# Optimization experiments

Hardware: AMD Instinct MI355X
Metric: run time of the kernel (lower is better)

Reference implementation:

```python
import jax, jax.numpy as jnp
import numpy as np

THETA = 10.0      # spike threshold
TAU_SR = 10.0     # synaptic (PSP) alpha-kernel time constant
TAU_REF = 1.0     # refractory alpha-kernel time constant
SCALE_REF = 2.0   # refractory scale (kernel = -scaleRef*theta*(t/tauRef)e^{1-t/tauRef})
TAU_RHO = 1.0     # surrogate-gradient width
SCALE_RHO = 1.0   # surrogate-gradient scale
TS = 1.0          # simulation step (ms)
E = 2.718281828459045

@jax.custom_vjp
def spike_surrogate(u):
    return (u >= THETA).astype(u.dtype)

def _spike_fwd(u):
    return (u >= THETA).astype(u.dtype), u

def _spike_bwd(u, g):
    # SLAYER surrogate spike-pdf gradient
    pdf = (SCALE_RHO / TAU_RHO) * jnp.exp(-jnp.abs(u - THETA) / TAU_RHO)
    return (g * pdf,)

spike_surrogate.defvjp(_spike_fwd, _spike_bwd)

def psp_spike(x):
    # x: (N, ..., T). PSP = causal temporal conv with alpha kernel
    # eps(t) = (t/tauSr) e^{1-t/tauSr}, realized EXACTLY as a 2-state IIR recursion.
    # spike = threshold; each emitted spike injects refractory alpha kernel
    # -scaleRef*theta*(t/tauRef) e^{1-t/tauRef} into the future membrane.
    xt = jnp.moveaxis(x, -1, 0)  # (T, ...)
    a_sr = jnp.exp(jnp.asarray(-TS / TAU_SR, x.dtype))
    a_rf = jnp.exp(jnp.asarray(-TS / TAU_REF, x.dtype))
    c_sr = E / TAU_SR
    c_rf = -SCALE_REF * THETA * E / TAU_REF
    z = jnp.zeros_like(xt[0])
    def step(carry, xi):
        gp, hp, gr, hr = carry
        hp = a_sr * (hp + gp)
        gp = a_sr * gp + xi
        hr = a_rf * (hr + gr)   # same recursion over past spikes
        gr = a_rf * gr
        u = c_sr * hp + c_rf * hr  # membrane = PSP + refractory
        s = spike_surrogate(u)
        return (gp, hp, gr + s, hr), s
    _, st = jax.lax.scan(step, (z, z, z, z), xt)
    return jnp.moveaxis(st, 0, -1)

def sum_pool(x, k):
    # SLAYER pool: conv with constant weight 1.1*theta over kxk window, stride k
    N, C, H, W, T = x.shape
    xs = x.reshape(N, C, H // k, k, W // k, k, T).sum(axis=(3, 5))
    return 1.1 * THETA * xs

def conv2dt(x, w, pad):
    # SLAYER conv = conv3d with kernel (k,k,1): per-time-step 2D conv, T as trailing dim
    return jax.lax.conv_general_dilated(
        x, w[..., None], (1, 1, 1),
        [(pad, pad), (pad, pad), (0, 0)],
        dimension_numbers=('NCHWT', 'OIHWT', 'NCHWT'))

def forward(s_in, w1, w2, w3, w4a, w4b):
    x = psp_spike(sum_pool(s_in, 4))              # (N,2,32,32,T)
    x = psp_spike(conv2dt(x, w1, 2))              # (N,32,32,32,T)
    x = psp_spike(sum_pool(x, 2))                 # (N,32,16,16,T)
    x = psp_spike(conv2dt(x, w2, 1))              # (N,64,16,16,T)
    x = psp_spike(sum_pool(x, 2))                 # (N,64,8,8,T)
    x = psp_spike(conv2dt(x, w3, 1))              # (N,64,8,8,T)
    N, T = x.shape[0], x.shape[-1]
    xf = x.reshape(N, -1, T)                      # (N, 64*8*8, T)
    x = psp_spike(jnp.einsum('nft,of->not', xf, w4a))  # (N,256,T)
    x = psp_spike(jnp.einsum('nct,oc->not', x, w4b))   # (N,11,T)
    return x

def setup_inputs():
    key = jax.random.key(0)
    ks = jax.random.split(key, 6)
    N, T = 4, 300
    # Bernoulli(0.05) event spikes, DVS128 gesture format (N,2,128,128,T)
    s_in = (jax.random.uniform(ks[0], (N, 2, 128, 128, T)) < 0.05).astype(jnp.float32)
    w1 = jax.random.normal(ks[1], (32, 2, 5, 5), jnp.float32) * 10.0 * 0.05   # weightScale=10
    w2 = jax.random.normal(ks[2], (64, 32, 3, 3), jnp.float32) * 20.0 * 0.01  # weightScale=20
    w3 = jax.random.normal(ks[3], (64, 64, 3, 3), jnp.float32) * 20.0 * 0.01  # weightScale=20
    w4a = jax.random.normal(ks[4], (256, 64 * 8 * 8), jnp.float32) * 0.01
    w4b = jax.random.normal(ks[5], (11, 256), jnp.float32) * 0.05
    return {"s_in": s_in, "w1": w1, "w2": w2, "w3": w3, "w4a": w4a, "w4b": w4b}

def reference(s_in, w1, w2, w3, w4a, w4b):
    return forward(s_in, w1, w2, w3, w4a, w4b)
```

## Files before the change

kernel.cpp:

```cpp
#include <hip/hip_runtime.h>
#include <cstdint>

#define TT 300
#define TC 75
#define NBATCH 4

typedef float pf2 __attribute__((ext_vector_type(2)));
typedef _Float16 h8t __attribute__((ext_vector_type(8)));
typedef float f32x4 __attribute__((ext_vector_type(4)));

__device__ __forceinline__ void psp_step(float z, float& gp, float& hp, float& gr, float& hr, float& s_out) {
    hp = 0.90483741803595957f * (hp + gp);
    gp = 0.90483741803595957f * gp + z;
    hr = 0.36787944117144233f * (hr + gr);
    gr = 0.36787944117144233f * gr;
    float u = 0.27182818284590452f * hp + (-54.365636569180904f) * hr;
    float s = (u >= 10.0f) ? 1.0f : 0.0f;
    gr += s;
    s_out = s;
}

template <int R>
__global__ void k_scan_redp(const float* __restrict__ z, float* __restrict__ s,
                            int n_neur, int pstride) {
    int i = blockIdx.x * 64 + threadIdx.x;
    if (i >= n_neur) return;
    const float* zp = z + (size_t)i * TT;
    float* sp = s + (size_t)i * TT;
    float gp = 0.f, hp = 0.f, gr = 0.f, hr = 0.f;
#pragma unroll 1
    for (int c = 0; c < 25; ++c) {
        const float* p = zp + c * 12;
        float4 a0 = *(const float4*)(p);
        float4 a1 = *(const float4*)(p + 4);
        float4 a2 = *(const float4*)(p + 8);
#pragma unroll
        for (int r = 1; r < R; ++r) {
            const float* pr = p + (size_t)r * pstride;
            float4 b0 = *(const float4*)(pr);
            float4 b1 = *(const float4*)(pr + 4);
            float4 b2 = *(const float4*)(pr + 8);
            a0.x += b0.x; a0.y += b0.y; a0.z += b0.z; a0.w += b0.w;
            a1.x += b1.x; a1.y += b1.y; a1.z += b1.z; a1.w += b1.w;
            a2.x += b2.x; a2.y += b2.y; a2.z += b2.z; a2.w += b2.w;
        }
        float4 o0, o1, o2;
        psp_step(a0.x, gp, hp, gr, hr, o0.x);
        psp_step(a0.y, gp, hp, gr, hr, o0.y);
        psp_step(a0.z, gp, hp, gr, hr, o0.z);
        psp_step(a0.w, gp, hp, gr, hr, o0.w);
        psp_step(a1.x, gp, hp, gr, hr, o1.x);
        psp_step(a1.y, gp, hp, gr, hr, o1.y);
        psp_step(a1.z, gp, hp, gr, hr, o1.z);
        psp_step(a1.w, gp, hp, gr, hr, o1.w);
        psp_step(a2.x, gp, hp, gr, hr, o2.x);
        psp_step(a2.y, gp, hp, gr, hr, o2.y);
        psp_step(a2.z, gp, hp, gr, hr, o2.z);
        psp_step(a2.w, gp, hp, gr, hr, o2.w);
        float* q = sp + c * 12;
        *(float4*)(q) = o0;
        *(float4*)(q + 4) = o1;
        *(float4*)(q + 8) = o2;
    }
}

__global__ void k_scan16_f16(const float* __restrict__ z, _Float16* __restrict__ s16) {
    int i = blockIdx.x * 64 + threadIdx.x;
    int n = i >> 12, f = i & 4095;
    const float* zp = z + (size_t)i * 16;
    _Float16* sp = s16 + ((size_t)n * TT) * 4096 + f;
    float gp = 0.f, hp = 0.f, gr = 0.f, hr = 0.f;
#define SC16_CHUNK(TCI, NTT) do {                                              \
    const float* pp = zp + (size_t)(TCI) * (16384 * 16);                       \
    float4 a0 = *(const float4*)(pp);                                          \
    float4 a1 = *(const float4*)(pp + 4);                                      \
    float4 a2 = *(const float4*)(pp + 8);                                      \
    float4 a3 = *(const float4*)(pp + 12);                                     \
    float zv[16] = {a0.x,a0.y,a0.z,a0.w,a1.x,a1.y,a1.z,a1.w,                   \
                    a2.x,a2.y,a2.z,a2.w,a3.x,a3.y,a3.z,a3.w};                  \
    _Pragma("unroll")                                                          \
    for (int tt = 0; tt < (NTT); ++tt) {                                       \
        float o;                                                               \
        psp_step(zv[tt], gp, hp, gr, hr, o);                                   \
        sp[(size_t)((TCI) * 16 + tt) * 4096] = (_Float16)o;                    \
    }                                                                          \
} while (0)
#pragma unroll 1
    for (int tcc = 0; tcc < 18; ++tcc) SC16_CHUNK(tcc, 16);
    SC16_CHUNK(18, 12);
#undef SC16_CHUNK
}

template <int C, int H2, int W2>
__global__ void __launch_bounds__(256) k_spsq16(const float* __restrict__ z,
                                                _Float16* __restrict__ s16) {
    constexpr int H = 2 * H2, W = 2 * W2;
    constexpr int NP = NBATCH * C * H * W;
    constexpr int C8 = C / 8;
    __shared__ _Float16 tile[16 * C];

    int i = blockIdx.x * 256 + threadIdx.x;
    int q = i & 3;
    int p = i >> 2;
    int c  = p % C;
    int x2 = (p / C) % W2;
    int y2 = (p / (C * W2)) % H2;
    int n  = p / (C * W2 * H2);
    int dy = q >> 1, dx = q & 1;
    int pz = ((n * C + c) * H + 2 * y2 + dy) * W + 2 * x2 + dx;
    const float* zp = z + (size_t)pz * 16;

    int tid = threadIdx.x;
    int wt  = tid & 15;
    int wc8 = tid >> 4;
    int p0 = blockIdx.x * 64;
    int wx2 = (p0 / C) % W2;
    int wy2 = (p0 / (C * W2)) % H2;
    int wn  = p0 / (C * W2 * H2);
    _Float16* wbase = s16 + ((((size_t)(wn * C8 + wc8) * H2 + wy2) * W2 + wx2) * TT) * 8;

    float gp = 0.f, hp = 0.f, gr = 0.f, hr = 0.f;
    float Gp = 0.f, Hp = 0.f, Gr = 0.f, Hr = 0.f;
#define SPSQ_CHUNK(TCI, NTT) do {                                              \
    const float* pp = zp + (size_t)(TCI) * (NP * 16);                          \
    float4 a0 = *(const float4*)(pp);                                          \
    float4 a1 = *(const float4*)(pp + 4);                                      \
    float4 a2 = *(const float4*)(pp + 8);                                      \
    float4 a3 = *(const float4*)(pp + 12);                                     \
    float zv[16] = {a0.x,a0.y,a0.z,a0.w,a1.x,a1.y,a1.z,a1.w,                   \
                    a2.x,a2.y,a2.z,a2.w,a3.x,a3.y,a3.z,a3.w};                  \
    float ov[16];                                                              \
    _Pragma("unroll")                                                          \
    for (int tt = 0; tt < (NTT); ++tt) {                                       \
        float sq;                                                              \
        psp_step(zv[tt], gp, hp, gr, hr, sq);                                  \
        float t1 = sq + __shfl_xor(sq, 1, 64);                                 \
        float pool = t1 + __shfl_xor(t1, 2, 64);                               \
        psp_step(11.0f * pool, Gp, Hp, Gr, Hr, ov[tt]);                        \
    }                                                                          \
    __syncthreads();                                                           \
    if (q == 0) {                                                              \
        _Pragma("unroll")                                                      \
        for (int tt = 0; tt < (NTT); ++tt)                                     \
            tile[tt * C + c] = (_Float16)ov[tt];                               \
    }                                                                          \
    __syncthreads();                                                           \
    if (tid < 16 * C8 && wt < (NTT)) {                                         \
        h8t v = *(const h8t*)(tile + wt * C + wc8 * 8);                        \
        *(h8t*)(wbase + (size_t)((TCI) * 16 + wt) * 8) = v;                    \
    }                                                                          \
} while (0)
#pragma unroll 1
    for (int tcc = 0; tcc < 18; ++tcc) SPSQ_CHUNK(tcc, 16);
    SPSQ_CHUNK(18, 12);
#undef SPSQ_CHUNK
}

__device__ __forceinline__ void pack_wmfma_item(int i, const float* __restrict__ w,
                                                _Float16* __restrict__ wm, int CIN, int COUT) {
    int lane = i & 63;
    int r = i >> 6;
    int ver = r & 1; r >>= 1;
    int KC = CIN >> 5, CT = COUT >> 4;
    int ct = r % CT; r /= CT;
    int kc = r % KC;
    int tap = r / KC;
    int ky = tap / 3, kx = tap % 3;
    int co  = ct * 16 + (lane & 15);
    int ci0 = kc * 32 + (lane >> 4) * 8;
    _Float16 out[8];
#pragma unroll
    for (int j = 0; j < 8; ++j) {
        float wf = w[((co * CIN + ci0 + j) * 3 + ky) * 3 + kx];
        _Float16 hi = (_Float16)wf;
        out[j] = ver ? (_Float16)((wf - (float)hi) * 4096.0f) : hi;
    }
    *(h8t*)(wm + (size_t)i * 8) = *(h8t*)out;
}

__device__ __forceinline__ void pack_wfc_item(int i, const float* __restrict__ w,
                                              _Float16* __restrict__ wm, int FIN, int COUT) {
    int lane = i & 63;
    int r = i >> 6;
    int ver = r & 1; r >>= 1;
    int CT = COUT >> 4;
    int ct = r % CT;
    int kg = r / CT;
    int co = ct * 16 + (lane & 15);
    int f0 = kg * 32 + (lane >> 4) * 8;
    _Float16 out[8];
#pragma unroll
    for (int j = 0; j < 8; ++j) {
        float wf = w[(size_t)co * FIN + f0 + j];
        _Float16 hi = (_Float16)wf;
        out[j] = ver ? (_Float16)((wf - (float)hi) * 4096.0f) : hi;
    }
    *(h8t*)(wm + (size_t)i * 8) = *(h8t*)out;
}

__device__ __forceinline__ void pack_wl1_item(int i, const float* __restrict__ w,
                                              _Float16* __restrict__ wm) {
    int lane = i & 63;
    int r = i >> 6;
    int ver = r & 1;
    int ch = (r >> 1) & 1;
    int kc = r >> 2;
    int co = ch * 16 + (lane & 15);
    int k0 = kc * 32 + (lane >> 4) * 8;
    _Float16 out[8];
#pragma unroll
    for (int j = 0; j < 8; ++j) {
        int k = k0 + j;
        int ky = k >> 4, slot = k & 15, kx = slot >> 1, ci = slot & 1;
        float wf = (ky < 5 && kx < 5) ? w[((co * 2 + ci) * 5 + ky) * 5 + kx] : 0.f;
        _Float16 hif = (_Float16)wf;
        out[j] = ver ? (_Float16)((wf - (float)hif) * 4096.0f) : hif;
    }
    *(h8t*)(wm + (size_t)i * 8) = *(h8t*)out;
}

__global__ void k_pack_all(const float* __restrict__ w1, const float* __restrict__ w2,
                           const float* __restrict__ w3, const float* __restrict__ w4a,
                           _Float16* __restrict__ wl1m, _Float16* __restrict__ wm2,
                           _Float16* __restrict__ wm3, _Float16* __restrict__ wm4) {
    int i = blockIdx.x * 256 + threadIdx.x;
    if (i < 768)          pack_wl1_item(i, w1, wl1m);
    else if (i < 5376)    pack_wmfma_item(i - 768, w2, wm2, 32, 64);
    else if (i < 14592)   pack_wmfma_item(i - 5376, w3, wm3, 64, 64);
    else if (i < 276736)  pack_wfc_item(i - 14592, w4a, wm4, 4096, 256);
}

__global__ void k_pool4(const float* __restrict__ x, float* __restrict__ z) {
    int idx = blockIdx.x * 256 + threadIdx.x;
    if (idx >= NBATCH * 2 * 32 * 32 * TC) return;
    int tc = idx % TC;
    int p  = idx / TC;
    int w  = p % 32;
    int h  = (p / 32) % 32;
    int nc = p / (32 * 32);
    const float* base = x + (((size_t)nc * 128 + h * 4) * 128 + w * 4) * TT + tc * 4;
    float ax = 0.f, ay = 0.f, az = 0.f, aw = 0.f;
#pragma unroll
    for (int i = 0; i < 4; ++i)
#pragma unroll
        for (int j = 0; j < 4; ++j) {
            float4 v = *(const float4*)(base + ((size_t)i * 128 + j) * TT);
            ax += v.x; ay += v.y; az += v.z; aw += v.w;
        }
    float4 o; o.x = 11.0f * ax; o.y = 11.0f * ay; o.z = 11.0f * az; o.w = 11.0f * aw;
    *(float4*)(z + (size_t)p * TT + tc * 4) = o;
}

__global__ void __launch_bounds__(256, 2) k_l1_fused(const float* __restrict__ s0,
                                                     const _Float16* __restrict__ wl1,
                                                     _Float16* __restrict__ s2h) {
    constexpr int NT = 10;
    __shared__ _Float16 stage[7 * 32 * 42];
    __shared__ float    trans[256 * 33];
    __shared__ _Float16 tile[4 * 32 * 16];

    int bid = blockIdx.x;
    int y2 = bid & 15;
    int xh = (bid >> 4) & 3;
    int ch = (bid >> 6) & 1;
    int n  = bid >> 7;
    int tid = threadIdx.x;
    int lane = tid & 63;
    int wv = tid >> 6;
    int tl = lane & 15;
    int hi = lane >> 4;
    int yy = wv >> 1;
    int xq = wv & 1;

    int q     = tid & 3;
    int co_s  = (tid >> 2) & 15;
    int x2l_s = tid >> 6;
    int wt  = tid & 31;
    int wc8 = (tid >> 5) & 1;
    int wx  = tid >> 6;

    int tq = tid & 7;
    int lx = (tid >> 3) & 15;
    int ci = tid >> 7;
    int gx = xh * 8 + lx - 2;
    bool gxok = (gx >= 0 && gx < 32);
    size_t boff = (((size_t)(n * 2 + ci) * 32) * 32 + (gxok ? gx : 0)) * TT + tq * 4;
    int adr0 = (tq * 4) * 42 + lx * 2 + ci;

    const h8t* wv4 = (const h8t*)wl1;
    h8t wfr[3][2];
#pragma unroll
    for (int kc = 0; kc < 3; ++kc) {
        wfr[kc][0] = wv4[((kc * 2 + ch) * 2 + 0) * 64 + lane];
        wfr[kc][1] = wv4[((kc * 2 + ch) * 2 + 1) * 64 + lane];
    }

    float gp = 0.f, hp = 0.f, gr = 0.f, hr = 0.f;
    float Gp = 0.f, Hp = 0.f, Gr = 0.f, Hr = 0.f;

    float4 pf[7];
#pragma unroll
    for (int ii = 0; ii < 7; ++ii) {
        int gy = y2 * 2 + ii - 2;
        pf[ii] = make_float4(0.f, 0.f, 0.f, 0.f);
        if (gxok && gy >= 0 && gy < 32)
            pf[ii] = *(const float4*)(s0 + boff + (size_t)gy * (32 * TT));
    }

#pragma unroll 1
    for (int tc = 0; tc < NT; ++tc) {
#pragma unroll
        for (int ii = 0; ii < 7; ++ii) {
            int a = adr0 + ii * (32 * 42);
            stage[a + 0 * 42] = (_Float16)pf[ii].x;
            stage[a + 1 * 42] = (_Float16)pf[ii].y;
            stage[a + 2 * 42] = (_Float16)pf[ii].z;
            stage[a + 3 * 42] = (_Float16)pf[ii].w;
        }
        if (tc + 1 < NT) {
#pragma unroll
            for (int ii = 0; ii < 7; ++ii) {
                int gy = y2 * 2 + ii - 2;
                float4 v = make_float4(0.f, 0.f, 0.f, 0.f);
                if (gxok && gy >= 0 && gy < 32 && (tc + 1) * 32 + tq * 4 + 3 < TT)
                    v = *(const float4*)(s0 + boff + (size_t)gy * (32 * TT) + (tc + 1) * 32);
                pf[ii] = v;
            }
        }
        __syncthreads();
        f32x4 ah4[2][4], al4[2][4];
#pragma unroll
        for (int tg = 0; tg < 2; ++tg)
#pragma unroll
            for (int xi = 0; xi < 4; ++xi) {
                ah4[tg][xi] = (f32x4){0.f, 0.f, 0.f, 0.f};
                al4[tg][xi] = (f32x4){0.f, 0.f, 0.f, 0.f};
            }
#pragma unroll
        for (int kc = 0; kc < 3; ++kc) {
            int rowb = yy + 2 * kc + (hi >> 1);
#pragma unroll
            for (int tg = 0; tg < 2; ++tg) {
#pragma unroll
                for (int xi = 0; xi < 4; ++xi) {
                    int xo = xq * 4 + xi;
                    const uint32_t* lp = (const uint32_t*)(stage + (rowb * 32 + tg * 16 + tl) * 42 + xo * 2 + (hi & 1) * 8);
                    union { uint32_t u[4]; h8t h; } bu;
                    bu.u[0] = lp[0]; bu.u[1] = lp[1]; bu.u[2] = lp[2]; bu.u[3] = lp[3];
                    ah4[tg][xi] = __builtin_amdgcn_mfma_f32_16x16x32_f16(wfr[kc][0], bu.h, ah4[tg][xi], 0, 0, 0);
                    al4[tg][xi] = __builtin_amdgcn_mfma_f32_16x16x32_f16(wfr[kc][1], bu.h, al4[tg][xi], 0, 0, 0);
                }
            }
        }
#pragma unroll
        for (int tg = 0; tg < 2; ++tg)
#pragma unroll
            for (int xi = 0; xi < 4; ++xi) {
                int xo = xq * 4 + xi;
#pragma unroll
                for (int r = 0; r < 4; ++r) {
                    float u = ah4[tg][xi][r] + al4[tg][xi][r] * 2.44140625e-4f;
                    int rowt = ((xo >> 1) * 16 + hi * 4 + r) * 4 + yy * 2 + (xo & 1);
                    trans[rowt * 33 + tg * 16 + tl] = u;
                }
            }
        __syncthreads();
#pragma unroll
        for (int t = 0; t < 32; ++t) {
            float u = trans[tid * 33 + t];
            float sq;
            psp_step(u, gp, hp, gr, hr, sq);
            float t1 = sq + __shfl_xor(sq, 1, 64);
            float pool = t1 + __shfl_xor(t1, 2, 64);
            float ov;
            psp_step(11.0f * pool, Gp, Hp, Gr, Hr, ov);
            if (q == 0) tile[(x2l_s * 32 + t) * 16 + co_s] = (_Float16)ov;
        }
        __syncthreads();
        {
            int tg = tc * 32 + wt;
            if (tg < TT) {
                h8t v = *(const h8t*)(tile + (wx * 32 + wt) * 16 + wc8 * 8);
                int cg8 = ch * 2 + wc8;
                int x2g = xh * 4 + wx;
                *(h8t*)(s2h + ((((size_t)(n * 4 + cg8) * 16 + y2) * 16 + x2g) * (size_t)TT + tg) * 8) = v;
            }
        }
    }
}

template <int CIN, int COUT, int H, int W, int YPB, int XSPL>
__global__ void __launch_bounds__(256, 2) k_conv_mfma(const _Float16* __restrict__ s16,
                                                      const _Float16* __restrict__ wm,
                                                      float* __restrict__ z) {
    constexpr int NT = 19;
    constexpr int KC = CIN / 32;
    constexpr int CH = CIN / 8;
    constexpr int XW = W / XSPL;
    constexpr int XL = XW + 2;
    constexpr int CT = COUT / 16;
    constexpr int XPW = XW / 4;
    constexpr int ROWS = YPB + 2;
    constexpr int NP = NBATCH * COUT * H * W;
    __shared__ _Float16 lds[ROWS * XL * 16 * CIN];

    int bid = blockIdx.x;
    int tc = bid % NT;
    int r0 = bid / NT;
    int yb = (r0 % (H / YPB)) * YPB;
    r0 /= (H / YPB);
    int xh = r0 % XSPL;
    int n  = r0 / XSPL;
    int xb = xh * XW;
    int tid = threadIdx.x;

    constexpr int TOT = ROWS * XL * CH * 16;
    for (int i = tid; i < TOT; i += 256) {
        int t   = i & 15;
        int c   = (i >> 4) % CH;
        int xc  = ((i >> 4) / CH) % XL;
        int row = ((i >> 4) / CH) / XL;
        int tg = tc * 16 + t;
        int xi = xb + xc - 1;
        int yi = yb + row - 1;
        h8t v;
#pragma unroll
        for (int e = 0; e < 8; ++e) v[e] = (_Float16)0.0f;
        if (xi >= 0 && xi < W && yi >= 0 && yi < H && tg < TT)
            v = *(const h8t*)(s16 + ((((size_t)(n * CH + c) * H + yi) * W + xi) * TT + tg) * 8);
        int swz = (CIN == 32) ? ((t >> 1) & 3) : (t & 7);
        int off = ((row * XL + xc) * 16 + t) * CIN + ((c ^ swz) << 3);
        *(h8t*)(lds + off) = v;
    }
    __syncthreads();

    int lane = tid & 63;
    int wv   = tid >> 6;
    int tl   = lane & 15;
    int hi   = lane >> 4;
    const h8t* wmv = (const h8t*)wm;
    int swz = (CIN == 32) ? ((tl >> 1) & 3) : (tl & 7);

#pragma unroll
    for (int yy = 0; yy < YPB; ++yy) {
        f32x4 acc_h[XPW][CT], acc_l[XPW][CT];
#pragma unroll
        for (int a = 0; a < XPW; ++a)
#pragma unroll
            for (int b = 0; b < CT; ++b) {
                acc_h[a][b] = (f32x4){0.f, 0.f, 0.f, 0.f};
                acc_l[a][b] = (f32x4){0.f, 0.f, 0.f, 0.f};
            }
#pragma unroll
        for (int ky = 0; ky < 3; ++ky) {
#pragma unroll
            for (int kx = 0; kx < 3; ++kx) {
                int tap = ky * 3 + kx;
#pragma unroll
                for (int kc = 0; kc < KC; ++kc) {
                    h8t bf[XPW];
#pragma unroll
                    for (int xi = 0; xi < XPW; ++xi) {
                        int x = wv * XPW + xi;
                        int c = kc * 4 + hi;
                        int off = (((yy + ky) * XL + (x + kx)) * 16 + tl) * CIN + ((c ^ swz) << 3);
                        bf[xi] = *(const h8t*)(lds + off);
                    }
#pragma unroll
                    for (int ct = 0; ct < CT; ++ct) {
                        size_t wbase = ((size_t)(tap * KC + kc) * CT + ct) * 2;
                        h8t ah = wmv[(wbase + 0) * 64 + lane];
                        h8t al = wmv[(wbase + 1) * 64 + lane];
#pragma unroll
                        for (int xi = 0; xi < XPW; ++xi) {
                            acc_h[xi][ct] = __builtin_amdgcn_mfma_f32_16x16x32_f16(ah, bf[xi], acc_h[xi][ct], 0, 0, 0);
                            acc_l[xi][ct] = __builtin_amdgcn_mfma_f32_16x16x32_f16(al, bf[xi], acc_l[xi][ct], 0, 0, 0);
                        }
                    }
                }
            }
        }
#pragma unroll
        for (int xi = 0; xi < XPW; ++xi) {
            int x = xb + wv * XPW + xi;
#pragma unroll
            for (int ct = 0; ct < CT; ++ct) {
#pragma unroll
                for (int r = 0; r < 4; ++r) {
                    int co = ct * 16 + hi * 4 + r;
                    int pz = ((n * COUT + co) * H + (yb + yy)) * W + x;
                    z[((size_t)tc * NP + pz) * 16 + tl]
                        = acc_h[xi][ct][r] + acc_l[xi][ct][r] * 2.44140625e-4f;
                }
            }
        }
    }
}

template <int FIN, int OUT>
__global__ void __launch_bounds__(256) k_fc_mfma(const _Float16* __restrict__ s16,
                                                 const _Float16* __restrict__ wm,
                                                 float* __restrict__ z) {
    constexpr int NT = 19;
    constexpr int CT = OUT / 16;
    constexpr int KCH = 512;
    constexpr int NK = FIN / KCH;
    __shared__ _Float16 lds[KCH * 16];

    int bid = blockIdx.x;
    int tc = bid % NT;
    int n  = (bid / NT) % NBATCH;
    int cg = bid / (NT * NBATCH);
    int tid = threadIdx.x;
    int lane = tid & 63, wv = tid >> 6;
    int tl = lane & 15, hi = lane >> 4;
    int ct = cg * 4 + wv;

    f32x4 acc_h = (f32x4){0.f, 0.f, 0.f, 0.f};
    f32x4 acc_l = (f32x4){0.f, 0.f, 0.f, 0.f};
    const h8t* wmv = (const h8t*)wm;

    for (int kb = 0; kb < NK; ++kb) {
        __syncthreads();
#pragma unroll
        for (int j = 0; j < 4; ++j) {
            int chunk = tid + j * 256;
            int c = chunk & 63;
            int t = chunk >> 6;
            int tg = tc * 16 + t;
            h8t v;
#pragma unroll
            for (int e = 0; e < 8; ++e) v[e] = (_Float16)0.0f;
            if (tg < TT) v = *(const h8t*)(s16 + ((size_t)(n * TT + tg) * FIN + kb * KCH + c * 8));
            *(h8t*)(lds + ((t * 64 + (c ^ (t & 7))) << 3)) = v;
        }
        __syncthreads();
#pragma unroll
        for (int kc = 0; kc < KCH / 32; ++kc) {
            int c = kc * 4 + hi;
            h8t bf = *(const h8t*)(lds + ((tl * 64 + (c ^ (tl & 7))) << 3));
            size_t wbase = ((size_t)((kb * (KCH / 32) + kc) * CT + ct)) * 2;
            h8t ah = wmv[(wbase + 0) * 64 + lane];
            h8t al = wmv[(wbase + 1) * 64 + lane];
            acc_h = __builtin_amdgcn_mfma_f32_16x16x32_f16(ah, bf, acc_h, 0, 0, 0);
            acc_l = __builtin_amdgcn_mfma_f32_16x16x32_f16(al, bf, acc_l, 0, 0, 0);
        }
    }
    int tg = tc * 16 + tl;
    if (tg < TT) {
#pragma unroll
        for (int r = 0; r < 4; ++r) {
            int co = ct * 16 + hi * 4 + r;
            z[(size_t)(n * OUT + co) * TT + tg] = acc_h[r] + acc_l[r] * 2.44140625e-4f;
        }
    }
}

template <int OUT, int FIN, int OPER, int FSPLIT>
__global__ void k_fc_a(const float* __restrict__ s, const float* __restrict__ wgt,
                       float* __restrict__ z) {
    constexpr int OG = OUT / OPER, FCH = FIN / FSPLIT;
    int idx = blockIdx.x * 256 + threadIdx.x;
    if (idx >= NBATCH * OG * TC * FSPLIT) return;
    int tc = idx % TC;
    int og = (idx / TC) % OG;
    int n  = (idx / (TC * OG)) % NBATCH;
    int sp = idx / (TC * OG * NBATCH);
    const float* sb = s + (size_t)n * FIN * TT + (size_t)sp * FCH * TT + tc * 4;
    const float* wb = wgt + (size_t)sp * FCH;
    pf2 acc[OPER][2];
#pragma unroll
    for (int k = 0; k < OPER; ++k) { acc[k][0] = (pf2){0.f, 0.f}; acc[k][1] = (pf2){0.f, 0.f}; }
#pragma unroll 2
    for (int f = 0; f < FCH; f += 4) {
        float4 s0 = *(const float4*)(sb + (size_t)(f + 0) * TT);
        float4 s1 = *(const float4*)(sb + (size_t)(f + 1) * TT);
        float4 s2 = *(const float4*)(sb + (size_t)(f + 2) * TT);
        float4 s3 = *(const float4*)(sb + (size_t)(f + 3) * TT);
        pf2 s0a = {s0.x, s0.y}, s0b = {s0.z, s0.w};
        pf2 s1a = {s1.x, s1.y}, s1b = {s1.z, s1.w};
        pf2 s2a = {s2.x, s2.y}, s2b = {s2.z, s2.w};
        pf2 s3a = {s3.x, s3.y}, s3b = {s3.z, s3.w};
#pragma unroll
        for (int k = 0; k < OPER; ++k) {
            float4 wv = *(const float4*)(wb + (size_t)(og * OPER + k) * FIN + f);
            pf2 wx = {wv.x, wv.x}, wy = {wv.y, wv.y}, wz = {wv.z, wv.z}, ww = {wv.w, wv.w};
            pf2 a0 = acc[k][0], a1 = acc[k][1];
            a0 = __builtin_elementwise_fma(wx, s0a, a0);
            a0 = __builtin_elementwise_fma(wy, s1a, a0);
            a0 = __builtin_elementwise_fma(wz, s2a, a0);
            a0 = __builtin_elementwise_fma(ww, s3a, a0);
            a1 = __builtin_elementwise_fma(wx, s0b, a1);
            a1 = __builtin_elementwise_fma(wy, s1b, a1);
            a1 = __builtin_elementwise_fma(wz, s2b, a1);
            a1 = __builtin_elementwise_fma(ww, s3b, a1);
            acc[k][0] = a0; acc[k][1] = a1;
        }
    }
#pragma unroll
    for (int k = 0; k < OPER; ++k) {
        float4 o;
        o.x = acc[k][0].x; o.y = acc[k][0].y; o.z = acc[k][1].x; o.w = acc[k][1].y;
        *(float4*)(z + ((size_t)sp * NBATCH * OUT + (size_t)n * OUT + og * OPER + k) * TT + tc * 4) = o;
    }
}

extern "C" void kernel_launch(void* const* d_in, const int* in_sizes, int n_in,
                              void* d_out, int out_size, void* d_ws, size_t ws_size,
                              hipStream_t stream) {
    const float* s_in = (const float*)d_in[0];
    const float* w1   = (const float*)d_in[1];
    const float* w2   = (const float*)d_in[2];
    const float* w3   = (const float*)d_in[3];
    const float* w4a  = (const float*)d_in[4];
    const float* w4b  = (const float*)d_in[5];
    float* out = (float*)d_out;

    float* Z  = (float*)d_ws;
    float* Sb = Z + 39321600;
    float* WP = Sb + 9830400;
    _Float16* wm2 = (_Float16*)(WP + 1600);
    _Float16* wm3 = (_Float16*)(WP + 1600 + 18432);
    _Float16* S16 = (_Float16*)(Z + 25000000);
    _Float16* wm4 = (_Float16*)(Z + 28000000);
    _Float16* wl1m = (_Float16*)(Z + 30000000);
    float* s0 = Sb;
    _Float16* s2h = (_Float16*)(Sb + 2500000);
    _Float16* s4h = (_Float16*)(Sb + 5000000);

    auto g = [](int n) { return (n + 255) / 256; };
    auto g64 = [](int n) { return (n + 63) / 64; };

    k_pack_all<<<g(276736), 256, 0, stream>>>(w1, w2, w3, w4a, wl1m, wm2, wm3, wm4);

    k_pool4<<<g(614400), 256, 0, stream>>>(s_in, Z);
    k_scan_redp<1><<<g64(8192), 64, 0, stream>>>(Z, s0, 8192, 0);

    k_l1_fused<<<512, 256, 0, stream>>>(s0, wl1m, s2h);

    k_conv_mfma<32, 64, 16, 16, 2, 2><<<1216, 256, 0, stream>>>(s2h, wm2, Z);
    k_spsq16<64, 8, 8><<<256, 256, 0, stream>>>(Z, s4h);

    k_conv_mfma<64, 64, 8, 8, 1, 2><<<1216, 256, 0, stream>>>(s4h, wm3, Z);
    k_scan16_f16<<<256, 64, 0, stream>>>(Z, S16);

    k_fc_mfma<4096, 256><<<304, 256, 0, stream>>>(S16, wm4, Z);
    k_scan_redp<1><<<g64(1024), 64, 0, stream>>>(Z, Sb, 1024, 0);

    k_fc_a<11, 256, 1, 1><<<g(3300), 256, 0, stream>>>(Sb, w4b, Z);
    k_scan_redp<1><<<1, 64, 0, stream>>>(Z, out, 44, 0);
}
```

Before: 518.4 us.

## Merge pool and weight-pack kernels, shrink LDS stride, retune conv2 grid

Combines the sum-pool and the weight-packing kernels into a single launch, using block ranges to split the two jobs, which saves one kernel launch. It also changes the layer-1 staging LDS row stride from 42 to 34 halves to alter the bank mapping and cut shared memory, and doubles the conv2 MFMA grid through a template parameter change. The grid change and the stride change carry some risk of occupancy or bank-conflict regressions.

Measured after the change: 518.8 us. Within noise of the previous version (+0.1%).

```diff
diff --git a/kernel.cpp b/kernel.cpp
--- a/kernel.cpp
+++ b/kernel.cpp
@@ -219,43 +219,44 @@
     *(h8t*)(wm + (size_t)i * 8) = *(h8t*)out;
 }
 
-__global__ void k_pack_all(const float* __restrict__ w1, const float* __restrict__ w2,
-                           const float* __restrict__ w3, const float* __restrict__ w4a,
-                           _Float16* __restrict__ wl1m, _Float16* __restrict__ wm2,
-                           _Float16* __restrict__ wm3, _Float16* __restrict__ wm4) {
-    int i = blockIdx.x * 256 + threadIdx.x;
-    if (i < 768)          pack_wl1_item(i, w1, wl1m);
-    else if (i < 5376)    pack_wmfma_item(i - 768, w2, wm2, 32, 64);
-    else if (i < 14592)   pack_wmfma_item(i - 5376, w3, wm3, 64, 64);
-    else if (i < 276736)  pack_wfc_item(i - 14592, w4a, wm4, 4096, 256);
-}
-
-__global__ void k_pool4(const float* __restrict__ x, float* __restrict__ z) {
-    int idx = blockIdx.x * 256 + threadIdx.x;
-    if (idx >= NBATCH * 2 * 32 * 32 * TC) return;
-    int tc = idx % TC;
-    int p  = idx / TC;
-    int w  = p % 32;
-    int h  = (p / 32) % 32;
-    int nc = p / (32 * 32);
-    const float* base = x + (((size_t)nc * 128 + h * 4) * 128 + w * 4) * TT + tc * 4;
-    float ax = 0.f, ay = 0.f, az = 0.f, aw = 0.f;
-#pragma unroll
-    for (int i = 0; i < 4; ++i)
-#pragma unroll
-        for (int j = 0; j < 4; ++j) {
-            float4 v = *(const float4*)(base + ((size_t)i * 128 + j) * TT);
-            ax += v.x; ay += v.y; az += v.z; aw += v.w;
-        }
-    float4 o; o.x = 11.0f * ax; o.y = 11.0f * ay; o.z = 11.0f * az; o.w = 11.0f * aw;
-    *(float4*)(z + (size_t)p * TT + tc * 4) = o;
+__global__ void k_front(const float* __restrict__ x, float* __restrict__ z,
+                        const float* __restrict__ w1, const float* __restrict__ w2,
+                        const float* __restrict__ w3, const float* __restrict__ w4a,
+                        _Float16* __restrict__ wl1m, _Float16* __restrict__ wm2,
+                        _Float16* __restrict__ wm3, _Float16* __restrict__ wm4) {
+    if (blockIdx.x < 2400) {
+        int idx = blockIdx.x * 256 + threadIdx.x;
+        int tc = idx % TC;
+        int p  = idx / TC;
+        int w  = p % 32;
+        int h  = (p / 32) % 32;
+        int nc = p / (32 * 32);
+        const float* base = x + (((size_t)nc * 128 + h * 4) * 128 + w * 4) * TT + tc * 4;
+        float ax = 0.f, ay = 0.f, az = 0.f, aw = 0.f;
+#pragma unroll
+        for (int i = 0; i < 4; ++i)
+#pragma unroll
+            for (int j = 0; j < 4; ++j) {
+                float4 v = *(const float4*)(base + ((size_t)i * 128 + j) * TT);
+                ax += v.x; ay += v.y; az += v.z; aw += v.w;
+            }
+        float4 o; o.x = 11.0f * ax; o.y = 11.0f * ay; o.z = 11.0f * az; o.w = 11.0f * aw;
+        *(float4*)(z + (size_t)p * TT + tc * 4) = o;
+    } else {
+        int i = (blockIdx.x - 2400) * 256 + threadIdx.x;
+        if (i < 768)          pack_wl1_item(i, w1, wl1m);
+        else if (i < 5376)    pack_wmfma_item(i - 768, w2, wm2, 32, 64);
+        else if (i < 14592)   pack_wmfma_item(i - 5376, w3, wm3, 64, 64);
+        else if (i < 276736)  pack_wfc_item(i - 14592, w4a, wm4, 4096, 256);
+    }
 }
 
 __global__ void __launch_bounds__(256, 2) k_l1_fused(const float* __restrict__ s0,
                                                      const _Float16* __restrict__ wl1,
                                                      _Float16* __restrict__ s2h) {
     constexpr int NT = 10;
-    __shared__ _Float16 stage[7 * 32 * 42];
+    constexpr int SS = 34;
+    __shared__ _Float16 stage[7 * 32 * SS];
     __shared__ float    trans[256 * 33];
     __shared__ _Float16 tile[4 * 32 * 16];
 
@@ -285,7 +286,7 @@
     int gx = xh * 8 + lx - 2;
     bool gxok = (gx >= 0 && gx < 32);
     size_t boff = (((size_t)(n * 2 + ci) * 32) * 32 + (gxok ? gx : 0)) * TT + tq * 4;
-    int adr0 = (tq * 4) * 42 + lx * 2 + ci;
+    int adr0 = (tq * 4) * SS + lx * 2 + ci;
 
     const h8t* wv4 = (const h8t*)wl1;
     h8t wfr[3][2];
@@ -311,11 +312,11 @@
     for (int tc = 0; tc < NT; ++tc) {
 #pragma unroll
         for (int ii = 0; ii < 7; ++ii) {
-            int a = adr0 + ii * (32 * 42);
-            stage[a + 0 * 42] = (_Float16)pf[ii].x;
-            stage[a + 1 * 42] = (_Float16)pf[ii].y;
-            stage[a + 2 * 42] = (_Float16)pf[ii].z;
-            stage[a + 3 * 42] = (_Float16)pf[ii].w;
+            int a = adr0 + ii * (32 * SS);
+            stage[a + 0 * SS] = (_Float16)pf[ii].x;
+            stage[a + 1 * SS] = (_Float16)pf[ii].y;
+            stage[a + 2 * SS] = (_Float16)pf[ii].z;
+            stage[a + 3 * SS] = (_Float16)pf[ii].w;
         }
         if (tc + 1 < NT) {
 #pragma unroll
@@ -344,7 +345,7 @@
 #pragma unroll
                 for (int xi = 0; xi < 4; ++xi) {
                     int xo = xq * 4 + xi;
-                    const uint32_t* lp = (const uint32_t*)(stage + (rowb * 32 + tg * 16 + tl) * 42 + xo * 2 + (hi & 1) * 8);
+                    const uint32_t* lp = (const uint32_t*)(stage + (rowb * 32 + tg * 16 + tl) * SS + xo * 2 + (hi & 1) * 8);
                     union { uint32_t u[4]; h8t h; } bu;
                     bu.u[0] = lp[0]; bu.u[1] = lp[1]; bu.u[2] = lp[2]; bu.u[3] = lp[3];
                     ah4[tg][xi] = __builtin_amdgcn_mfma_f32_16x16x32_f16(wfr[kc][0], bu.h, ah4[tg][xi], 0, 0, 0);
@@ -628,17 +629,14 @@
     _Float16* s2h = (_Float16*)(Sb + 2500000);
     _Float16* s4h = (_Float16*)(Sb + 5000000);
 
-    auto g = [](int n) { return (n + 255) / 256; };
     auto g64 = [](int n) { return (n + 63) / 64; };
 
-    k_pack_all<<<g(276736), 256, 0, stream>>>(w1, w2, w3, w4a, wl1m, wm2, wm3, wm4);
-
-    k_pool4<<<g(614400), 256, 0, stream>>>(s_in, Z);
+    k_front<<<3481, 256, 0, stream>>>(s_in, Z, w1, w2, w3, w4a, wl1m, wm2, wm3, wm4);
     k_scan_redp<1><<<g64(8192), 64, 0, stream>>>(Z, s0, 8192, 0);
 
     k_l1_fused<<<512, 256, 0, stream>>>(s0, wl1m, s2h);
 
-    k_conv_mfma<32, 64, 16, 16, 2, 2><<<1216, 256, 0, stream>>>(s2h, wm2, Z);
+    k_conv_mfma<32, 64, 16, 16, 2, 4><<<2432, 256, 0, stream>>>(s2h, wm2, Z);
     k_spsq16<64, 8, 8><<<256, 256, 0, stream>>>(Z, s4h);
 
     k_conv_mfma<64, 64, 8, 8, 1, 2><<<1216, 256, 0, stream>>>(s4h, wm3, Z);
@@ -647,6 +645,6 @@
     k_fc_mfma<4096, 256><<<304, 256, 0, stream>>>(S16, wm4, Z);
     k_scan_redp<1><<<g64(1024), 64, 0, stream>>>(Z, Sb, 1024, 0);
 
-    k_fc_a<11, 256, 1, 1><<<g(3300), 256, 0, stream>>>(Sb, w4b, Z);
+    k_fc_a<11, 256, 1, 1><<<(3300 + 255) / 256, 256, 0, stream>>>(Sb, w4b, Z);
     k_scan_redp<1><<<1, 64, 0, stream>>>(Z, out, 44, 0);
 }
```
